# Kernel tuning notes

Hardware: AMD Instinct MI355X
Metric: run time of the kernel (lower is better)

The kernel has to match this reference:

```python
import jax, jax.numpy as jnp
import numpy as np

N_NODES = 100000
N_EDGES = 1600000
IN_DIM = 256
OUT_DIM = 128


def setup_inputs() -> dict:
    key = jax.random.key(0)
    k1, k2, k3, k4, k5 = jax.random.split(key, 5)
    x = jax.random.normal(k1, (N_NODES, IN_DIM), dtype=jnp.float32)
    W = jax.random.normal(k2, (OUT_DIM, IN_DIM), dtype=jnp.float32) * (1.0 / np.sqrt(IN_DIM))
    edge_row = jax.random.randint(k3, (N_EDGES,), 0, N_NODES, dtype=jnp.int32)
    edge_col = jax.random.randint(k4, (N_EDGES,), 0, N_NODES, dtype=jnp.int32)
    # normalized adjacency values (positive, like D^-1/2 A D^-1/2 entries)
    edge_val = jax.random.uniform(k5, (N_EDGES,), dtype=jnp.float32)
    return {"x": x, "W": W, "edge_row": edge_row, "edge_col": edge_col, "edge_val": edge_val}


def reference(x, W, edge_row, edge_col, edge_val):
    # h = x @ W.T  (Linear without bias), shape [N, out_dim]
    h = jnp.einsum('ni,oi->no', x, W)
    # SpMM: out[r] = sum_{e: row[e]==r} val[e] * h[col[e]]
    msgs = h[edge_col] * edge_val[:, None]           # [E, out_dim] irregular gather
    out = jax.ops.segment_sum(msgs, edge_row, num_segments=x.shape[0])
    return out
```

## Files before the change

kernel.cpp:

```cpp
#include <hip/hip_runtime.h>
#include <hip/hip_fp16.h>

#define N_NODES 100000
#define N_EDGES 1600000
#define IN_DIM  256
#define OUT_DIM 128

#define BROWS  512
#define NBKT   196
#define CAP    9216
#define CHUNK  8192
#define NBLK   196
#define DCAP   12288

#define BMT    32
#define NTILE  (N_NODES / BMT)
#define TPB    4
#define NGBLK  ((NTILE + TPB - 1) / TPB)

typedef __attribute__((ext_vector_type(8))) short short8;
typedef __attribute__((ext_vector_type(4))) float f32x4;
typedef __attribute__((ext_vector_type(2))) float f32x2;

__device__ __forceinline__ unsigned short f2bf(float f) {
    unsigned int u = __float_as_uint(f);
    u += 0x7FFFu + ((u >> 16) & 1u);
    return (unsigned short)(u >> 16);
}
__device__ __forceinline__ float bf2f(unsigned int u16) {
    return __uint_as_float(u16 << 16);
}

__device__ __forceinline__ short8 pack8(float4 a, float4 b) {
    short8 s;
    s[0] = (short)f2bf(a.x); s[1] = (short)f2bf(a.y);
    s[2] = (short)f2bf(a.z); s[3] = (short)f2bf(a.w);
    s[4] = (short)f2bf(b.x); s[5] = (short)f2bf(b.y);
    s[6] = (short)f2bf(b.z); s[7] = (short)f2bf(b.w);
    return s;
}

__global__ __launch_bounds__(256) void w_to_bf16(const float* __restrict__ W,
                                                 unsigned short* __restrict__ Wb) {
    int i = blockIdx.x * 256 + threadIdx.x;
    if (i < OUT_DIM * IN_DIM) Wb[i] = f2bf(W[i]);
}

__global__ __launch_bounds__(512) void gemm_bin(const float* __restrict__ x,
                                                const unsigned short* __restrict__ Wb,
                                                unsigned short* __restrict__ hb,
                                                const int* __restrict__ erow,
                                                const int* __restrict__ ecol,
                                                const float* __restrict__ eval,
                                                int* __restrict__ bcnt,
                                                int2* __restrict__ gbuf) {
    __shared__ unsigned short xs[2 * BMT * 256];
    const int tid = threadIdx.x;

    if (blockIdx.x < NBLK) {
        int* h    = (int*)xs;
        int* gpos = h + NBKT;
        int* rcur = gpos + NBKT;
        for (int i = tid; i < NBKT; i += 512) { h[i] = 0; rcur[i] = 0; }
        __syncthreads();
        const int e0 = blockIdx.x * CHUNK;
        for (int i = tid; i < CHUNK; i += 512) {
            int e = e0 + i;
            if (e < N_EDGES) atomicAdd(&h[erow[e] >> 9], 1);
        }
        __syncthreads();
        for (int i = tid; i < NBKT; i += 512)
            gpos[i] = h[i] ? (i * CAP + atomicAdd(&bcnt[i], h[i])) : 0;
        __syncthreads();
        for (int i = tid; i < CHUNK; i += 512) {
            int e = e0 + i;
            if (e < N_EDGES) {
                int r = erow[e];
                int b = r >> 9;
                unsigned int vb  = __half_as_ushort(__float2half(eval[e]));
                unsigned int rec = (vb << 17) | (unsigned int)ecol[e];
                int pos = gpos[b] + atomicAdd(&rcur[b], 1);
                gbuf[pos] = make_int2((int)rec, r);
            }
        }
        return;
    }

    const int g    = blockIdx.x - NBLK;
    const int t0   = g * TPB;
    const int wid  = tid >> 6;
    const int lane = tid & 63;
    const int l15  = lane & 15;
    const int g8   = (lane >> 4) * 8;
    const int col  = wid * 16 + l15;
    const int sw   = (l15 & 7) << 4;
    char* lb = (char*)xs;

    const int srow = tid >> 4;
    const int scs  = (tid & 15) * 16;
    const int swr  = (srow & 7) << 4;
    const int wb0  = (srow * 512 + (scs + 0) * 2) ^ swr;
    const int wb1  = (srow * 512 + (scs + 8) * 2) ^ swr;

    short8 bfr[8];
    const unsigned short* wrow = Wb + (size_t)col * IN_DIM + g8;
#pragma unroll
    for (int kk = 0; kk < 8; ++kk)
        bfr[kk] = *(const short8*)(wrow + kk * 32);

    {
        const int ti = t0;
        const int gr = (ti < NTILE) ? (ti * BMT + srow) : srow;
        const float4* src = (const float4*)(x + (size_t)gr * IN_DIM + scs);
        float4 f0 = src[0], f1 = src[1], f2 = src[2], f3 = src[3];
        *(short8*)(lb + wb0) = pack8(f0, f1);
        *(short8*)(lb + wb1) = pack8(f2, f3);
    }

#pragma unroll
    for (int i = 0; i < TPB; ++i) {
        float4 q0, q1, q2, q3;
        if (i + 1 < TPB) {
            const int ti = t0 + i + 1;
            const int gr = (ti < NTILE) ? (ti * BMT + srow) : srow;
            const float4* src = (const float4*)(x + (size_t)gr * IN_DIM + scs);
            q0 = src[0]; q1 = src[1]; q2 = src[2]; q3 = src[3];
        }
        __syncthreads();

        const int ti = t0 + i;
        const char* cb = lb + (i & 1) * (BMT * 512);
        short8 a0[8], a1[8];
#pragma unroll
        for (int kk = 0; kk < 8; ++kk) {
            a0[kk] = *(const short8*)(cb + ((l15 * 512 + (kk * 32 + g8) * 2) ^ sw));
            a1[kk] = *(const short8*)(cb + (((l15 + 16) * 512 + (kk * 32 + g8) * 2) ^ sw));
        }
        f32x4 acc0 = {0.f, 0.f, 0.f, 0.f}, acc1 = {0.f, 0.f, 0.f, 0.f};
#pragma unroll
        for (int kk = 0; kk < 8; ++kk) {
            acc0 = __builtin_amdgcn_mfma_f32_16x16x32_bf16(a0[kk], bfr[kk], acc0, 0, 0, 0);
            acc1 = __builtin_amdgcn_mfma_f32_16x16x32_bf16(a1[kk], bfr[kk], acc1, 0, 0, 0);
        }
        if (ti < NTILE) {
            const int rb0 = ti * BMT + (lane >> 4) * 4;
            const int rb1 = rb0 + 16;
#pragma unroll
            for (int q = 0; q < 4; ++q) {
                hb[(size_t)(rb0 + q) * OUT_DIM + col] = f2bf(acc0[q]);
                hb[(size_t)(rb1 + q) * OUT_DIM + col] = f2bf(acc1[q]);
            }
        }

        if (i + 1 < TPB) {
            char* wbuf = lb + ((i + 1) & 1) * (BMT * 512);
            *(short8*)(wbuf + wb0) = pack8(q0, q1);
            *(short8*)(wbuf + wb1) = pack8(q2, q3);
        }
    }
}

__global__ __launch_bounds__(256) void sort_bucket(const int2* __restrict__ gbuf,
                                                   const int* __restrict__ bcnt,
                                                   unsigned int* __restrict__ gcsr,
                                                   int* __restrict__ offs,
                                                   int* __restrict__ bend) {
    __shared__ int rh[BROWS], rc[BROWS];
    __shared__ int tmp[256];
    __shared__ unsigned int lout[DCAP];
    const int b    = blockIdx.x;
    const int base = b * CAP;
    const int cnt  = bcnt[b];
    const int r0   = b * BROWS;
    const int t    = threadIdx.x;

    rh[2 * t] = 0; rh[2 * t + 1] = 0;
    __syncthreads();
    for (int i = t; i < cnt; i += 256)
        atomicAdd(&rh[gbuf[base + i].y - r0], 1);
    __syncthreads();

    int a0 = rh[2 * t], a1 = rh[2 * t + 1], s = a0 + a1;
    tmp[t] = s;
    __syncthreads();
    for (int d = 1; d < 256; d <<= 1) {
        int a = (t >= d) ? tmp[t - d] : 0;
        __syncthreads();
        tmp[t] += a;
        __syncthreads();
    }
    int ex = tmp[t] - s;
    rc[2 * t]     = ex;
    rc[2 * t + 1] = ex + a0;
    offs[r0 + 2 * t]     = base + ex;
    offs[r0 + 2 * t + 1] = base + ex + a0;
    if (t == 0) bend[b] = base + cnt;
    __syncthreads();

    if (cnt <= DCAP) {
        for (int i = t; i < cnt; i += 256) {
            int2 rr = gbuf[base + i];
            int p = atomicAdd(&rc[rr.y - r0], 1);
            lout[p] = (unsigned int)rr.x;
        }
        __syncthreads();
        for (int i = t; i < cnt; i += 256)
            gcsr[base + i] = lout[i];
    } else {
        for (int i = t; i < cnt; i += 256) {
            int2 rr = gbuf[base + i];
            int p = atomicAdd(&rc[rr.y - r0], 1);
            gcsr[base + p] = (unsigned int)rr.x;
        }
    }
}

__global__ __launch_bounds__(256) void spmm_gather(const unsigned short* __restrict__ hb,
                                                   const int* __restrict__ offs,
                                                   const int* __restrict__ bend,
                                                   const unsigned int* __restrict__ ccv,
                                                   float* __restrict__ out) {
    const int lane = threadIdx.x & 63;
    const int half = lane >> 5;
    const int li   = lane & 31;
    const int r    = blockIdx.x * 8 + (threadIdx.x >> 6) * 2 + half;

    const int js = offs[r];
    const int je = ((r & (BROWS - 1)) == (BROWS - 1)) ? bend[r >> 9] : offs[r + 1];

    f32x2 accA = {0.f, 0.f}, accB = {0.f, 0.f};
    for (int j = js; __any(j < je); j += 8) {
        unsigned int e[8];
        uint2 p[8];
#pragma unroll
        for (int q = 0; q < 8; ++q) {
            int jj = j + q;
            e[q] = ccv[jj < je ? jj : 0];
        }
#pragma unroll
        for (int q = 0; q < 8; ++q)
            p[q] = *(const uint2*)(hb + (size_t)(e[q] & 0x1FFFFu) * OUT_DIM + li * 4);
#pragma unroll
        for (int q = 0; q < 8; ++q) {
            float v = (j + q < je)
                    ? __half2float(__ushort_as_half((unsigned short)(e[q] >> 17)))
                    : 0.f;
            f32x2 vv  = {v, v};
            f32x2 h01 = { __uint_as_float(p[q].x << 16),
                          __uint_as_float(p[q].x & 0xFFFF0000u) };
            f32x2 h23 = { __uint_as_float(p[q].y << 16),
                          __uint_as_float(p[q].y & 0xFFFF0000u) };
            accA = __builtin_elementwise_fma(vv, h01, accA);
            accB = __builtin_elementwise_fma(vv, h23, accB);
        }
    }
    float4 o = {accA.x, accA.y, accB.x, accB.y};
    *(float4*)(out + (size_t)r * OUT_DIM + li * 4) = o;
}

__global__ __launch_bounds__(512) void gemm_plain(const float* __restrict__ x,
                                                  const float* __restrict__ W,
                                                  unsigned short* __restrict__ hb) {
    __shared__ unsigned short xs[2 * BMT * 256];
    const int tid = threadIdx.x;
    const int m0  = blockIdx.x * (2 * BMT);
    char* lb = (char*)xs;
    {
        const int row = tid >> 3;
        const int cs  = (tid & 7) * 32;
        const int gr  = m0 + row;
        if (gr < N_NODES) {
            const float4* src = (const float4*)(x + (size_t)gr * IN_DIM + cs);
#pragma unroll
            for (int i = 0; i < 4; ++i) {
                float4 a = src[2 * i], b = src[2 * i + 1];
                int byt = (row * 512 + (cs + 8 * i) * 2) ^ ((row & 7) << 4);
                *(short8*)(lb + byt) = pack8(a, b);
            }
        } else {
            short8 z = {0, 0, 0, 0, 0, 0, 0, 0};
#pragma unroll
            for (int i = 0; i < 4; ++i) {
                int byt = (row * 512 + (cs + 8 * i) * 2) ^ ((row & 7) << 4);
                *(short8*)(lb + byt) = z;
            }
        }
    }
    __syncthreads();
    const int wid  = tid >> 6;
    const int lane = tid & 63;
    const int l15  = lane & 15;
    const int g8   = (lane >> 4) * 8;
    short8 bfr[8];
    const float* wrowf = W + (size_t)(wid * 16 + l15) * IN_DIM + g8;
#pragma unroll
    for (int kk = 0; kk < 8; ++kk) {
        float4 wa = *(const float4*)(wrowf + kk * 32);
        float4 wb = *(const float4*)(wrowf + kk * 32 + 4);
        bfr[kk] = pack8(wa, wb);
    }
    const int col = wid * 16 + l15;
    const int sw  = (l15 & 7) << 4;
    const char* lbc = (const char*)xs;
#pragma unroll
    for (int rp = 0; rp < 2; ++rp) {
        const int r0 = rp * 32 + l15;
        const int r1 = r0 + 16;
        short8 a0[8], a1[8];
#pragma unroll
        for (int kk = 0; kk < 8; ++kk) {
            a0[kk] = *(const short8*)(lbc + ((r0 * 512 + (kk * 32 + g8) * 2) ^ sw));
            a1[kk] = *(const short8*)(lbc + ((r1 * 512 + (kk * 32 + g8) * 2) ^ sw));
        }
        f32x4 acc0 = {0.f, 0.f, 0.f, 0.f}, acc1 = {0.f, 0.f, 0.f, 0.f};
#pragma unroll
        for (int kk = 0; kk < 8; ++kk) {
            acc0 = __builtin_amdgcn_mfma_f32_16x16x32_bf16(a0[kk], bfr[kk], acc0, 0, 0, 0);
            acc1 = __builtin_amdgcn_mfma_f32_16x16x32_bf16(a1[kk], bfr[kk], acc1, 0, 0, 0);
        }
        const int rb0 = m0 + rp * 32 + (lane >> 4) * 4;
        const int rb1 = rb0 + 16;
#pragma unroll
        for (int i = 0; i < 4; ++i) {
            if (rb0 + i < N_NODES) hb[(size_t)(rb0 + i) * OUT_DIM + col] = f2bf(acc0[i]);
            if (rb1 + i < N_NODES) hb[(size_t)(rb1 + i) * OUT_DIM + col] = f2bf(acc1[i]);
        }
    }
}

__global__ __launch_bounds__(256) void spmm_scatter(const unsigned short* __restrict__ hb,
                                                    const int* __restrict__ erow,
                                                    const int* __restrict__ ecol,
                                                    const float* __restrict__ eval,
                                                    float* __restrict__ out) {
    const int lane = threadIdx.x & 63;
    const int eloc = threadIdx.x >> 6;
    const int stride = gridDim.x * 4;
    for (int e = blockIdx.x * 4 + eloc; e < N_EDGES; e += stride) {
        const int r = erow[e];
        const int c = ecol[e];
        const float v = eval[e];
        unsigned int p = *(const unsigned int*)(hb + (size_t)c * OUT_DIM + lane * 2);
        float* o = out + (size_t)r * OUT_DIM + lane * 2;
        unsafeAtomicAdd(o + 0, v * bf2f(p & 0xFFFFu));
        unsafeAtomicAdd(o + 1, v * bf2f(p >> 16));
    }
}

extern "C" void kernel_launch(void* const* d_in, const int* in_sizes, int n_in,
                              void* d_out, int out_size, void* d_ws, size_t ws_size,
                              hipStream_t stream) {
    const float* x    = (const float*)d_in[0];
    const float* W    = (const float*)d_in[1];
    const int*   erow = (const int*)d_in[2];
    const int*   ecol = (const int*)d_in[3];
    const float* eval = (const float*)d_in[4];
    float*       out  = (float*)d_out;

    const size_t H_ELEMS = (size_t)N_NODES * OUT_DIM;
    unsigned short* hb    = (unsigned short*)d_ws;
    int2*           gbuf  = (int2*)(hb + H_ELEMS);
    unsigned int*   gcsr  = (unsigned int*)(gbuf + NBKT * CAP);
    int*            offs  = (int*)(gcsr + NBKT * CAP);
    int*            bend  = offs + NBKT * BROWS + 8;
    int*            bcnt  = bend + NBKT;
    unsigned short* Wb    = (unsigned short*)(bcnt + NBKT + 8);
    const size_t need = ((char*)(Wb + OUT_DIM * IN_DIM)) - (char*)d_ws;

    if (ws_size >= need) {
        hipMemsetAsync(bcnt, 0, NBKT * sizeof(int), stream);
        w_to_bf16<<<(OUT_DIM * IN_DIM + 255) / 256, 256, 0, stream>>>(W, Wb);
        gemm_bin<<<NBLK + NGBLK, 512, 0, stream>>>(x, Wb, hb, erow, ecol, eval, bcnt, gbuf);
        sort_bucket<<<NBKT, 256, 0, stream>>>(gbuf, bcnt, gcsr, offs, bend);
        spmm_gather<<<N_NODES / 8, 256, 0, stream>>>(hb, offs, bend, gcsr, out);
    } else {
        gemm_plain<<<(N_NODES + 2 * BMT - 1) / (2 * BMT), 512, 0, stream>>>(x, W, hb);
        hipMemsetAsync(d_out, 0, (size_t)out_size * sizeof(float), stream);
        spmm_scatter<<<8192, 256, 0, stream>>>(hb, erow, ecol, eval, out);
    }
}
```

Measured before the change: 126.3 us.

## Use one 32-row tile per 256-thread GEMM block with two column groups per wave

The fused GEMM/binning kernel drops its 4-tile-per-block double-buffered pipeline. Each 256-thread block now handles one 32-row tile, and each wave computes two 16-column groups, so it holds twice the W fragments and issues twice the MFMAs per A load. This raises grid parallelism and halves LDS per block, and the binning blocks now run with 256 threads. The cost is losing the prefetch overlap and reloading W once per tile in every block. The fallback gemm_plain path is reshaped the same way.

```diff
diff --git a/kernel.cpp b/kernel.cpp
--- a/kernel.cpp
+++ b/kernel.cpp
@@ -15,8 +15,6 @@
 
 #define BMT    32
 #define NTILE  (N_NODES / BMT)
-#define TPB    4
-#define NGBLK  ((NTILE + TPB - 1) / TPB)
 
 typedef __attribute__((ext_vector_type(8))) short short8;
 typedef __attribute__((ext_vector_type(4))) float f32x4;
@@ -46,7 +44,7 @@
     if (i < OUT_DIM * IN_DIM) Wb[i] = f2bf(W[i]);
 }
 
-__global__ __launch_bounds__(512) void gemm_bin(const float* __restrict__ x,
+__global__ __launch_bounds__(256) void gemm_bin(const float* __restrict__ x,
                                                 const unsigned short* __restrict__ Wb,
                                                 unsigned short* __restrict__ hb,
                                                 const int* __restrict__ erow,
@@ -54,25 +52,25 @@
                                                 const float* __restrict__ eval,
                                                 int* __restrict__ bcnt,
                                                 int2* __restrict__ gbuf) {
-    __shared__ unsigned short xs[2 * BMT * 256];
+    __shared__ unsigned short xs[BMT * 256];
     const int tid = threadIdx.x;
 
     if (blockIdx.x < NBLK) {
         int* h    = (int*)xs;
         int* gpos = h + NBKT;
         int* rcur = gpos + NBKT;
-        for (int i = tid; i < NBKT; i += 512) { h[i] = 0; rcur[i] = 0; }
+        for (int i = tid; i < NBKT; i += 256) { h[i] = 0; rcur[i] = 0; }
         __syncthreads();
         const int e0 = blockIdx.x * CHUNK;
-        for (int i = tid; i < CHUNK; i += 512) {
+        for (int i = tid; i < CHUNK; i += 256) {
             int e = e0 + i;
             if (e < N_EDGES) atomicAdd(&h[erow[e] >> 9], 1);
         }
         __syncthreads();
-        for (int i = tid; i < NBKT; i += 512)
+        for (int i = tid; i < NBKT; i += 256)
             gpos[i] = h[i] ? (i * CAP + atomicAdd(&bcnt[i], h[i])) : 0;
         __syncthreads();
-        for (int i = tid; i < CHUNK; i += 512) {
+        for (int i = tid; i < CHUNK; i += 256) {
             int e = e0 + i;
             if (e < N_EDGES) {
                 int r = erow[e];
@@ -86,77 +84,66 @@
         return;
     }
 
-    const int g    = blockIdx.x - NBLK;
-    const int t0   = g * TPB;
+    const int m0 = (blockIdx.x - NBLK) * BMT;
+    char* lb = (char*)xs;
+
+    {
+        const int row = tid >> 3;
+        const int cs  = (tid & 7) * 32;
+        const float4* src = (const float4*)(x + (size_t)(m0 + row) * IN_DIM + cs);
+        float4 f0 = src[0], f1 = src[1], f2 = src[2], f3 = src[3];
+        float4 f4 = src[4], f5 = src[5], f6 = src[6], f7 = src[7];
+        const int sb = (row & 7) << 4;
+        *(short8*)(lb + ((row * 512 + (cs + 0)  * 2) ^ sb)) = pack8(f0, f1);
+        *(short8*)(lb + ((row * 512 + (cs + 8)  * 2) ^ sb)) = pack8(f2, f3);
+        *(short8*)(lb + ((row * 512 + (cs + 16) * 2) ^ sb)) = pack8(f4, f5);
+        *(short8*)(lb + ((row * 512 + (cs + 24) * 2) ^ sb)) = pack8(f6, f7);
+    }
+    __syncthreads();
+
     const int wid  = tid >> 6;
     const int lane = tid & 63;
     const int l15  = lane & 15;
     const int g8   = (lane >> 4) * 8;
-    const int col  = wid * 16 + l15;
+    const int c0   = wid * 16;
+    const int c1   = c0 + 64;
     const int sw   = (l15 & 7) << 4;
-    char* lb = (char*)xs;
-
-    const int srow = tid >> 4;
-    const int scs  = (tid & 15) * 16;
-    const int swr  = (srow & 7) << 4;
-    const int wb0  = (srow * 512 + (scs + 0) * 2) ^ swr;
-    const int wb1  = (srow * 512 + (scs + 8) * 2) ^ swr;
-
-    short8 bfr[8];
-    const unsigned short* wrow = Wb + (size_t)col * IN_DIM + g8;
-#pragma unroll
-    for (int kk = 0; kk < 8; ++kk)
-        bfr[kk] = *(const short8*)(wrow + kk * 32);
-
-    {
-        const int ti = t0;
-        const int gr = (ti < NTILE) ? (ti * BMT + srow) : srow;
-        const float4* src = (const float4*)(x + (size_t)gr * IN_DIM + scs);
-        float4 f0 = src[0], f1 = src[1], f2 = src[2], f3 = src[3];
-        *(short8*)(lb + wb0) = pack8(f0, f1);
-        *(short8*)(lb + wb1) = pack8(f2, f3);
-    }
-
-#pragma unroll
-    for (int i = 0; i < TPB; ++i) {
-        float4 q0, q1, q2, q3;
-        if (i + 1 < TPB) {
-            const int ti = t0 + i + 1;
-            const int gr = (ti < NTILE) ? (ti * BMT + srow) : srow;
-            const float4* src = (const float4*)(x + (size_t)gr * IN_DIM + scs);
-            q0 = src[0]; q1 = src[1]; q2 = src[2]; q3 = src[3];
-        }
-        __syncthreads();
-
-        const int ti = t0 + i;
-        const char* cb = lb + (i & 1) * (BMT * 512);
-        short8 a0[8], a1[8];
-#pragma unroll
-        for (int kk = 0; kk < 8; ++kk) {
-            a0[kk] = *(const short8*)(cb + ((l15 * 512 + (kk * 32 + g8) * 2) ^ sw));
-            a1[kk] = *(const short8*)(cb + (((l15 + 16) * 512 + (kk * 32 + g8) * 2) ^ sw));
-        }
-        f32x4 acc0 = {0.f, 0.f, 0.f, 0.f}, acc1 = {0.f, 0.f, 0.f, 0.f};
-#pragma unroll
-        for (int kk = 0; kk < 8; ++kk) {
-            acc0 = __builtin_amdgcn_mfma_f32_16x16x32_bf16(a0[kk], bfr[kk], acc0, 0, 0, 0);
-            acc1 = __builtin_amdgcn_mfma_f32_16x16x32_bf16(a1[kk], bfr[kk], acc1, 0, 0, 0);
-        }
-        if (ti < NTILE) {
-            const int rb0 = ti * BMT + (lane >> 4) * 4;
-            const int rb1 = rb0 + 16;
-#pragma unroll
-            for (int q = 0; q < 4; ++q) {
-                hb[(size_t)(rb0 + q) * OUT_DIM + col] = f2bf(acc0[q]);
-                hb[(size_t)(rb1 + q) * OUT_DIM + col] = f2bf(acc1[q]);
-            }
-        }
-
-        if (i + 1 < TPB) {
-            char* wbuf = lb + ((i + 1) & 1) * (BMT * 512);
-            *(short8*)(wbuf + wb0) = pack8(q0, q1);
-            *(short8*)(wbuf + wb1) = pack8(q2, q3);
-        }
+    const char* lbc = (const char*)xs;
+
+    short8 b0[8], b1[8];
+    const unsigned short* w0 = Wb + (size_t)(c0 + l15) * IN_DIM + g8;
+    const unsigned short* w1 = Wb + (size_t)(c1 + l15) * IN_DIM + g8;
+#pragma unroll
+    for (int kk = 0; kk < 8; ++kk) {
+        b0[kk] = *(const short8*)(w0 + kk * 32);
+        b1[kk] = *(const short8*)(w1 + kk * 32);
+    }
+
+    short8 a0[8], a1[8];
+#pragma unroll
+    for (int kk = 0; kk < 8; ++kk) {
+        a0[kk] = *(const short8*)(lbc + ((l15 * 512 + (kk * 32 + g8) * 2) ^ sw));
+        a1[kk] = *(const short8*)(lbc + (((l15 + 16) * 512 + (kk * 32 + g8) * 2) ^ sw));
+    }
+
+    f32x4 acc00 = {0.f, 0.f, 0.f, 0.f}, acc10 = {0.f, 0.f, 0.f, 0.f};
+    f32x4 acc01 = {0.f, 0.f, 0.f, 0.f}, acc11 = {0.f, 0.f, 0.f, 0.f};
+#pragma unroll
+    for (int kk = 0; kk < 8; ++kk) {
+        acc00 = __builtin_amdgcn_mfma_f32_16x16x32_bf16(a0[kk], b0[kk], acc00, 0, 0, 0);
+        acc10 = __builtin_amdgcn_mfma_f32_16x16x32_bf16(a1[kk], b0[kk], acc10, 0, 0, 0);
+        acc01 = __builtin_amdgcn_mfma_f32_16x16x32_bf16(a0[kk], b1[kk], acc01, 0, 0, 0);
+        acc11 = __builtin_amdgcn_mfma_f32_16x16x32_bf16(a1[kk], b1[kk], acc11, 0, 0, 0);
+    }
+
+    const int rb0 = m0 + (lane >> 4) * 4;
+    const int rb1 = rb0 + 16;
+#pragma unroll
+    for (int q = 0; q < 4; ++q) {
+        hb[(size_t)(rb0 + q) * OUT_DIM + c0 + l15] = f2bf(acc00[q]);
+        hb[(size_t)(rb1 + q) * OUT_DIM + c0 + l15] = f2bf(acc10[q]);
+        hb[(size_t)(rb0 + q) * OUT_DIM + c1 + l15] = f2bf(acc01[q]);
+        hb[(size_t)(rb1 + q) * OUT_DIM + c1 + l15] = f2bf(acc11[q]);
     }
 }
 
@@ -258,73 +245,66 @@
     *(float4*)(out + (size_t)r * OUT_DIM + li * 4) = o;
 }
 
-__global__ __launch_bounds__(512) void gemm_plain(const float* __restrict__ x,
+__global__ __launch_bounds__(256) void gemm_plain(const float* __restrict__ x,
                                                   const float* __restrict__ W,
                                                   unsigned short* __restrict__ hb) {
-    __shared__ unsigned short xs[2 * BMT * 256];
+    __shared__ unsigned short xs[BMT * 256];
     const int tid = threadIdx.x;
-    const int m0  = blockIdx.x * (2 * BMT);
+    const int m0  = blockIdx.x * BMT;
     char* lb = (char*)xs;
     {
         const int row = tid >> 3;
         const int cs  = (tid & 7) * 32;
-        const int gr  = m0 + row;
-        if (gr < N_NODES) {
-            const float4* src = (const float4*)(x + (size_t)gr * IN_DIM + cs);
-#pragma unroll
-            for (int i = 0; i < 4; ++i) {
-                float4 a = src[2 * i], b = src[2 * i + 1];
-                int byt = (row * 512 + (cs + 8 * i) * 2) ^ ((row & 7) << 4);
-                *(short8*)(lb + byt) = pack8(a, b);
-            }
-        } else {
-            short8 z = {0, 0, 0, 0, 0, 0, 0, 0};
-#pragma unroll
-            for (int i = 0; i < 4; ++i) {
-                int byt = (row * 512 + (cs + 8 * i) * 2) ^ ((row & 7) << 4);
-                *(short8*)(lb + byt) = z;
-            }
-        }
+        const float4* src = (const float4*)(x + (size_t)(m0 + row) * IN_DIM + cs);
+        float4 f0 = src[0], f1 = src[1], f2 = src[2], f3 = src[3];
+        float4 f4 = src[4], f5 = src[5], f6 = src[6], f7 = src[7];
+        const int sb = (row & 7) << 4;
+        *(short8*)(lb + ((row * 512 + (cs + 0)  * 2) ^ sb)) = pack8(f0, f1);
+        *(short8*)(lb + ((row * 512 + (cs + 8)  * 2) ^ sb)) = pack8(f2, f3);
+        *(short8*)(lb + ((row * 512 + (cs + 16) * 2) ^ sb)) = pack8(f4, f5);
+        *(short8*)(lb + ((row * 512 + (cs + 24) * 2) ^ sb)) = pack8(f6, f7);
     }
     __syncthreads();
     const int wid  = tid >> 6;
     const int lane = tid & 63;
     const int l15  = lane & 15;
     const int g8   = (lane >> 4) * 8;
-    short8 bfr[8];
-    const float* wrowf = W + (size_t)(wid * 16 + l15) * IN_DIM + g8;
-#pragma unroll
-    for (int kk = 0; kk < 8; ++kk) {
-        float4 wa = *(const float4*)(wrowf + kk * 32);
-        float4 wb = *(const float4*)(wrowf + kk * 32 + 4);
-        bfr[kk] = pack8(wa, wb);
-    }
-    const int col = wid * 16 + l15;
-    const int sw  = (l15 & 7) << 4;
+    const int c0   = wid * 16;
+    const int c1   = c0 + 64;
+    const int sw   = (l15 & 7) << 4;
     const char* lbc = (const char*)xs;
-#pragma unroll
-    for (int rp = 0; rp < 2; ++rp) {
-        const int r0 = rp * 32 + l15;
-        const int r1 = r0 + 16;
-        short8 a0[8], a1[8];
-#pragma unroll
-        for (int kk = 0; kk < 8; ++kk) {
-            a0[kk] = *(const short8*)(lbc + ((r0 * 512 + (kk * 32 + g8) * 2) ^ sw));
-            a1[kk] = *(const short8*)(lbc + ((r1 * 512 + (kk * 32 + g8) * 2) ^ sw));
-        }
-        f32x4 acc0 = {0.f, 0.f, 0.f, 0.f}, acc1 = {0.f, 0.f, 0.f, 0.f};
-#pragma unroll
-        for (int kk = 0; kk < 8; ++kk) {
-            acc0 = __builtin_amdgcn_mfma_f32_16x16x32_bf16(a0[kk], bfr[kk], acc0, 0, 0, 0);
-            acc1 = __builtin_amdgcn_mfma_f32_16x16x32_bf16(a1[kk], bfr[kk], acc1, 0, 0, 0);
-        }
-        const int rb0 = m0 + rp * 32 + (lane >> 4) * 4;
-        const int rb1 = rb0 + 16;
-#pragma unroll
-        for (int i = 0; i < 4; ++i) {
-            if (rb0 + i < N_NODES) hb[(size_t)(rb0 + i) * OUT_DIM + col] = f2bf(acc0[i]);
-            if (rb1 + i < N_NODES) hb[(size_t)(rb1 + i) * OUT_DIM + col] = f2bf(acc1[i]);
-        }
+
+    short8 b0[8], b1[8];
+#pragma unroll
+    for (int kk = 0; kk < 8; ++kk) {
+        const float* wr0 = W + (size_t)(c0 + l15) * IN_DIM + g8 + kk * 32;
+        const float* wr1 = W + (size_t)(c1 + l15) * IN_DIM + g8 + kk * 32;
+        b0[kk] = pack8(*(const float4*)wr0, *(const float4*)(wr0 + 4));
+        b1[kk] = pack8(*(const float4*)wr1, *(const float4*)(wr1 + 4));
+    }
+    short8 a0[8], a1[8];
+#pragma unroll
+    for (int kk = 0; kk < 8; ++kk) {
+        a0[kk] = *(const short8*)(lbc + ((l15 * 512 + (kk * 32 + g8) * 2) ^ sw));
+        a1[kk] = *(const short8*)(lbc + (((l15 + 16) * 512 + (kk * 32 + g8) * 2) ^ sw));
+    }
+    f32x4 acc00 = {0.f, 0.f, 0.f, 0.f}, acc10 = {0.f, 0.f, 0.f, 0.f};
+    f32x4 acc01 = {0.f, 0.f, 0.f, 0.f}, acc11 = {0.f, 0.f, 0.f, 0.f};
+#pragma unroll
+    for (int kk = 0; kk < 8; ++kk) {
+        acc00 = __builtin_amdgcn_mfma_f32_16x16x32_bf16(a0[kk], b0[kk], acc00, 0, 0, 0);
+        acc10 = __builtin_amdgcn_mfma_f32_16x16x32_bf16(a1[kk], b0[kk], acc10, 0, 0, 0);
+        acc01 = __builtin_amdgcn_mfma_f32_16x16x32_bf16(a0[kk], b1[kk], acc01, 0, 0, 0);
+        acc11 = __builtin_amdgcn_mfma_f32_16x16x32_bf16(a1[kk], b1[kk], acc11, 0, 0, 0);
+    }
+    const int rb0 = m0 + (lane >> 4) * 4;
+    const int rb1 = rb0 + 16;
+#pragma unroll
+    for (int q = 0; q < 4; ++q) {
+        hb[(size_t)(rb0 + q) * OUT_DIM + c0 + l15] = f2bf(acc00[q]);
+        hb[(size_t)(rb1 + q) * OUT_DIM + c0 + l15] = f2bf(acc10[q]);
+        hb[(size_t)(rb0 + q) * OUT_DIM + c1 + l15] = f2bf(acc01[q]);
+        hb[(size_t)(rb1 + q) * OUT_DIM + c1 + l15] = f2bf(acc11[q]);
     }
 }
 
@@ -370,11 +350,11 @@
     if (ws_size >= need) {
         hipMemsetAsync(bcnt, 0, NBKT * sizeof(int), stream);
         w_to_bf16<<<(OUT_DIM * IN_DIM + 255) / 256, 256, 0, stream>>>(W, Wb);
-        gemm_bin<<<NBLK + NGBLK, 512, 0, stream>>>(x, Wb, hb, erow, ecol, eval, bcnt, gbuf);
+        gemm_bin<<<NBLK + NTILE, 256, 0, stream>>>(x, Wb, hb, erow, ecol, eval, bcnt, gbuf);
         sort_bucket<<<NBKT, 256, 0, stream>>>(gbuf, bcnt, gcsr, offs, bend);
         spmm_gather<<<N_NODES / 8, 256, 0, stream>>>(hb, offs, bend, gcsr, out);
     } else {
-        gemm_plain<<<(N_NODES + 2 * BMT - 1) / (2 * BMT), 512, 0, stream>>>(x, W, hb);
+        gemm_plain<<<NTILE, 256, 0, stream>>>(x, W, hb);
         hipMemsetAsync(d_out, 0, (size_t)out_size * sizeof(float), stream);
         spmm_scatter<<<8192, 256, 0, stream>>>(hb, erow, ecol, eval, out);
     }
```

Result: slower. 152.1 us (+20.5%).
